# Performance work log

Hardware: AMD Instinct MI355X
Metric: run time of the kernel (lower is better)

The kernel has to match this reference:

```python
import jax, jax.numpy as jnp
import numpy as np

DIM = 768
HEADS = 12
HEAD_DIM = DIM // HEADS
SCALE = HEAD_DIM ** -0.5


def setup_inputs() -> dict:
    key = jax.random.key(0)
    ks = jax.random.split(key, 6)
    B, N = 4, 2048
    x = jax.random.normal(ks[0], (B, N, DIM), dtype=jnp.float32)
    s = DIM ** -0.5
    Wq = jax.random.normal(ks[1], (DIM, DIM), dtype=jnp.float32) * s
    Wk = jax.random.normal(ks[2], (DIM, DIM), dtype=jnp.float32) * s
    Wv = jax.random.normal(ks[3], (DIM, DIM), dtype=jnp.float32) * s
    Wp = jax.random.normal(ks[4], (DIM, DIM), dtype=jnp.float32) * s
    bp = jnp.zeros((DIM,), dtype=jnp.float32)
    return {"x": x, "Wq": Wq, "Wk": Wk, "Wv": Wv, "Wp": Wp, "bp": bp}


def reference(x, Wq, Wk, Wv, Wp, bp):
    B, N, C = x.shape
    # separate Q/K/V linears (no bias, qkv_bias=False); torch Linear: x @ W.T
    q = (x @ Wq.T).reshape(B, N, HEADS, HEAD_DIM).transpose(0, 2, 1, 3)
    k = (x @ Wk.T).reshape(B, N, HEADS, HEAD_DIM).transpose(0, 2, 1, 3)
    v = (x @ Wv.T).reshape(B, N, HEADS, HEAD_DIM).transpose(0, 2, 1, 3)
    # explicit full [B,H,N,N] attention matrix, as in the source
    attn = jnp.einsum("bhqd,bhkd->bhqk", q, k) * SCALE
    attn = jax.nn.softmax(attn, axis=-1)
    out = jnp.einsum("bhqk,bhkd->bhqd", attn, v)
    out = out.transpose(0, 2, 1, 3).reshape(B, N, C)
    return out @ Wp.T + bp
```

## Files before the change

kernel.cpp:

```cpp
#include <hip/hip_runtime.h>
#include <cstdint>

#define DIM   768
#define HEADS 12
#define HDIM  64
#define BATCH 4
#define SEQ   2048
#define MROWS (BATCH*SEQ)

typedef __bf16 bf16;
typedef __bf16 bf16x4_t __attribute__((ext_vector_type(4)));
typedef __bf16 bf16x8_t __attribute__((ext_vector_type(8)));
typedef float  f32x4_t  __attribute__((ext_vector_type(4)));
typedef float  f32x16_t __attribute__((ext_vector_type(16)));
typedef unsigned int u32x4_t __attribute__((ext_vector_type(4)));
typedef unsigned int u32x2_t __attribute__((ext_vector_type(2)));

__global__ void cast_bf16_kernel(const float* __restrict__ src, bf16* __restrict__ dst, int n4) {
    int i = blockIdx.x * blockDim.x + threadIdx.x;
    if (i >= n4) return;
    const float4 v = reinterpret_cast<const float4*>(src)[i];
    bf16x4_t o;
    o[0] = (bf16)v.x; o[1] = (bf16)v.y; o[2] = (bf16)v.z; o[3] = (bf16)v.w;
    reinterpret_cast<bf16x4_t*>(dst)[i] = o;
}

__global__ void cast_w4_kernel(const float* __restrict__ s0, const float* __restrict__ s1,
                               const float* __restrict__ s2, const float* __restrict__ s3,
                               bf16* __restrict__ d0, bf16* __restrict__ d1,
                               bf16* __restrict__ d2, bf16* __restrict__ d3, int n4) {
    int i = blockIdx.x * blockDim.x + threadIdx.x;
    if (i >= n4) return;
    int y = blockIdx.y;
    const float* src = (y == 0) ? s0 : (y == 1) ? s1 : (y == 2) ? s2 : s3;
    bf16* dst        = (y == 0) ? d0 : (y == 1) ? d1 : (y == 2) ? d2 : d3;
    const float4 v = reinterpret_cast<const float4*>(src)[i];
    bf16x4_t o;
    o[0] = (bf16)v.x; o[1] = (bf16)v.y; o[2] = (bf16)v.z; o[3] = (bf16)v.w;
    reinterpret_cast<bf16x4_t*>(dst)[i] = o;
}

__device__ __forceinline__ void gload_lds16(const bf16* g, bf16* l) {
    __builtin_amdgcn_global_load_lds((const __attribute__((address_space(1))) void*)g,
                                     (__attribute__((address_space(3))) void*)l, 16, 0, 0);
}

__global__ __launch_bounds__(256, 3) void qkvv_gemm(
        const bf16* __restrict__ X,
        const bf16* __restrict__ Wq, const bf16* __restrict__ Wk, const bf16* __restrict__ Wv,
        bf16* __restrict__ Q, bf16* __restrict__ Kd, bf16* __restrict__ Vt)
{
    __shared__ __align__(16) bf16 SM[128 * 128];
    bf16* As = SM;
    bf16* Bs = SM + 128 * 64;
    const int tid  = threadIdx.x;

    const int d  = blockIdx.x + 6 * blockIdx.y + 384 * blockIdx.z;
    const int L  = (d & 7) * 144 + (d >> 3);
    const int z  = L / 384;
    const int rem = L % 384;
    const int m0 = (rem % 6) * 128;
    const int n0 = (rem / 6) * 128;

    const bf16* Ap = (z == 0) ? Wq : (z == 1 ? Wk : Wv);
    const int lane = tid & 63;
    const int w    = tid >> 6;
    const int wm   = (w & 1) * 64, wn = (w >> 1) * 64;
    const int lr   = lane & 15, quad = lane >> 4;

    f32x4_t acc[4][4] = {};

    for (int kk = 0; kk < DIM; kk += 64) {
        #pragma unroll
        for (int i = 0; i < 4; ++i) {
            int c = tid + i * 256;
            int row = c >> 3, ch = c & 7;
            int gch = ch ^ (row & 7);
            gload_lds16(Ap + (size_t)(m0 + row) * DIM + kk + gch * 8, &As[row * 64 + ch * 8]);
            gload_lds16(X  + (size_t)(n0 + row) * DIM + kk + gch * 8, &Bs[row * 64 + ch * 8]);
        }
        __syncthreads();
        #pragma unroll
        for (int ks = 0; ks < 2; ++ks) {
            bf16x8_t af[4], bfr[4];
            #pragma unroll
            for (int i = 0; i < 4; ++i) {
                int row = wm + i * 16 + lr;
                int ch = (ks * 4 + quad) ^ (row & 7);
                af[i] = *reinterpret_cast<const bf16x8_t*>(&As[row * 64 + ch * 8]);
            }
            #pragma unroll
            for (int j = 0; j < 4; ++j) {
                int row = wn + j * 16 + lr;
                int ch = (ks * 4 + quad) ^ (row & 7);
                bfr[j] = *reinterpret_cast<const bf16x8_t*>(&Bs[row * 64 + ch * 8]);
            }
            #pragma unroll
            for (int i = 0; i < 4; ++i)
                #pragma unroll
                for (int j = 0; j < 4; ++j)
                    acc[i][j] = __builtin_amdgcn_mfma_f32_16x16x32_bf16(af[i], bfr[j], acc[i][j], 0, 0, 0);
        }
        __syncthreads();
    }

    if (z == 2) {
        #pragma unroll
        for (int i = 0; i < 4; ++i) {
            int ml = wm + i * 16 + quad * 4;
            #pragma unroll
            for (int j = 0; j < 4; ++j) {
                int nl = wn + j * 16 + lr;
                #pragma unroll
                for (int r = 0; r < 4; ++r)
                    SM[(ml + r) * 128 + nl] = (bf16)acc[i][j][r];
            }
        }
        __syncthreads();
        const int rr = tid >> 4, cc = tid & 15;
        #pragma unroll
        for (int rnd = 0; rnd < 8; ++rnd) {
            int ml = rnd * 16 + rr;
            *reinterpret_cast<bf16x8_t*>(&Vt[(size_t)(m0 + ml) * MROWS + n0 + cc * 8]) =
                *reinterpret_cast<const bf16x8_t*>(&SM[ml * 128 + cc * 8]);
        }
    } else {
        const float sc = (z == 0) ? 0.18033688011112042f : 1.0f;
        bf16* dst = (z == 0) ? Q : Kd;
        #pragma unroll
        for (int i = 0; i < 4; ++i) {
            int mb = m0 + wm + i * 16 + quad * 4;
            int h  = mb >> 6, d0 = mb & 63;
            #pragma unroll
            for (int j = 0; j < 4; ++j) {
                int sample = n0 + wn + j * 16 + lr;
                int b = sample >> 11, srow = sample & 2047;
                bf16x4_t o;
                #pragma unroll
                for (int r = 0; r < 4; ++r)
                    o[r] = (bf16)(acc[i][j][r] * sc);
                *reinterpret_cast<bf16x4_t*>(
                    &dst[(((size_t)b * HEADS + h) * SEQ + srow) * HDIM + d0]) = o;
            }
        }
    }
}

__global__ __launch_bounds__(256, 4) void out_gemm(
        const bf16* __restrict__ A,
        const bf16* __restrict__ W,
        const float* __restrict__ bias,
        float* __restrict__ out)
{
    __shared__ __align__(16) bf16 As[64*64];
    __shared__ __align__(16) bf16 Bs[128*64];
    const int tid  = threadIdx.x;

    const int d  = blockIdx.x + 6 * blockIdx.y;
    const int L  = (d & 7) * 96 + (d >> 3);
    const int n0 = (L % 6) * 128;
    const int m0 = (L / 6) * 64;

    const int lane = tid & 63;
    const int w    = tid >> 6;
    const int wm   = (w & 1) * 32, wn = (w >> 1) * 64;
    const int lr   = lane & 15, quad = lane >> 4;

    f32x4_t acc[2][4] = {};

    for (int kk = 0; kk < DIM; kk += 64) {
        #pragma unroll
        for (int i = 0; i < 2; ++i) {
            int c = tid + i * 256;
            int row = c >> 3, ch = c & 7;
            int gch = ch ^ (row & 7);
            gload_lds16(A + (size_t)(m0 + row) * DIM + kk + gch * 8, &As[row * 64 + ch * 8]);
        }
        #pragma unroll
        for (int i = 0; i < 4; ++i) {
            int c = tid + i * 256;
            int row = c >> 3, ch = c & 7;
            int gch = ch ^ (row & 7);
            gload_lds16(W + (size_t)(n0 + row) * DIM + kk + gch * 8, &Bs[row * 64 + ch * 8]);
        }
        __syncthreads();
        #pragma unroll
        for (int ks = 0; ks < 2; ++ks) {
            bf16x8_t af[2], bfr[4];
            #pragma unroll
            for (int i = 0; i < 2; ++i) {
                int row = wm + i * 16 + lr;
                int ch = (ks * 4 + quad) ^ (row & 7);
                af[i] = *reinterpret_cast<const bf16x8_t*>(&As[row * 64 + ch * 8]);
            }
            #pragma unroll
            for (int j = 0; j < 4; ++j) {
                int row = wn + j * 16 + lr;
                int ch = (ks * 4 + quad) ^ (row & 7);
                bfr[j] = *reinterpret_cast<const bf16x8_t*>(&Bs[row * 64 + ch * 8]);
            }
            #pragma unroll
            for (int i = 0; i < 2; ++i)
                #pragma unroll
                for (int j = 0; j < 4; ++j)
                    acc[i][j] = __builtin_amdgcn_mfma_f32_16x16x32_bf16(af[i], bfr[j], acc[i][j], 0, 0, 0);
        }
        __syncthreads();
    }

    #pragma unroll
    for (int i = 0; i < 2; ++i) {
        int mbase = m0 + wm + i * 16 + quad * 4;
        #pragma unroll
        for (int j = 0; j < 4; ++j) {
            int n = n0 + wn + j * 16 + lr;
            float bv = bias[n];
            #pragma unroll
            for (int r = 0; r < 4; ++r) {
                int m = mbase + r;
                out[(size_t)m * DIM + n] = acc[i][j][r] + bv;
            }
        }
    }
}

__global__ __launch_bounds__(256, 3) void attn_kernel(
        const bf16* __restrict__ Q, const bf16* __restrict__ Kd,
        const bf16* __restrict__ Vt, bf16* __restrict__ Ab)
{
    __shared__ __align__(16) bf16 KV[2][2][64*64];

    const int tid  = threadIdx.x;

    const int dd = blockIdx.x + 16 * blockIdx.y;
    const int L  = (dd & 7) * 96 + (dd >> 3);
    const int bh = L >> 4;
    const int q0 = (L & 15) * 128;

    const int b    = bh / HEADS, h = bh % HEADS;
    const int lane = tid & 63, w = tid >> 6;
    const int l31  = lane & 31, hw = lane >> 5;
    const int wq   = w * 32;

    const size_t qkbase = (size_t)bh * SEQ * HDIM;
    const size_t vbase  = (size_t)h * HDIM * MROWS + (size_t)b * SEQ;

    const int src_row = tid >> 3, src_ch = tid & 7;
    const int src_gch = src_ch ^ (src_row & 7);
    const int src_row2 = (tid + 256) >> 3, src_ch2 = tid & 7;
    const int src_gch2 = src_ch2 ^ (src_row2 & 7);

    {
        bf16* Qst = &KV[1][0][0];
        #pragma unroll
        for (int i = 0; i < 4; ++i) {
            int c = tid + i * 256;
            int row = c >> 3, ch = c & 7;
            int gch = ch ^ (row & 7);
            gload_lds16(Q + qkbase + (size_t)(q0 + row) * HDIM + gch * 8, &Qst[row * 64 + ch * 8]);
        }
    }

    const bf16* kp1 = Kd + qkbase + (size_t)src_row  * HDIM + src_gch  * 8;
    const bf16* kp2 = Kd + qkbase + (size_t)src_row2 * HDIM + src_gch2 * 8;
    const bf16* vp1 = Vt + vbase  + (size_t)src_row  * MROWS + src_gch  * 8;
    const bf16* vp2 = Vt + vbase  + (size_t)src_row2 * MROWS + src_gch2 * 8;
    bf16* kl1 = &KV[0][0][src_row  * 64 + src_ch  * 8];
    bf16* kl2 = &KV[0][0][src_row2 * 64 + src_ch2 * 8];
    bf16* vl1 = &KV[0][1][src_row  * 64 + src_ch  * 8];
    bf16* vl2 = &KV[0][1][src_row2 * 64 + src_ch2 * 8];
    const ptrdiff_t kstep = 64 * HDIM, vstep = 64;
    const ptrdiff_t lstep = 2 * 64 * 64;

    gload_lds16(kp1, kl1); gload_lds16(kp2, kl2);
    gload_lds16(vp1, vl1); gload_lds16(vp2, vl2);
    __syncthreads();

    bf16x8_t qf[4];
    {
        const bf16* Qst = &KV[1][0][0];
        int row = wq + l31;
        #pragma unroll
        for (int g = 0; g < 4; ++g) {
            int ch = (2 * g + hw) ^ (row & 7);
            qf[g] = *reinterpret_cast<const bf16x8_t*>(&Qst[row * 64 + ch * 8]);
        }
    }
    __syncthreads();

    f32x16_t oacc[2] = {};
    f32x16_t rsacc  = {};
    bf16x8_t ones8;
    #pragma unroll
    for (int i = 0; i < 8; ++i) ones8[i] = (bf16)1.0f;

    for (int it = 0; it < SEQ / 64; ++it) {
        const int buf = it & 1;
        if (it + 1 < SEQ / 64) {
            const ptrdiff_t g = (ptrdiff_t)(it + 1);
            const ptrdiff_t l = (buf ^ 1) ? lstep : 0;
            gload_lds16(kp1 + g * kstep, kl1 + l); gload_lds16(kp2 + g * kstep, kl2 + l);
            gload_lds16(vp1 + g * vstep, vl1 + l); gload_lds16(vp2 + g * vstep, vl2 + l);
        }

        const bf16* Ks = &KV[buf][0][0];
        const bf16* Vs = &KV[buf][1][0];

        f32x16_t sacc[2] = {};
        __builtin_amdgcn_s_setprio(1);
        #pragma unroll
        for (int kc = 0; kc < 2; ++kc) {
            int row = kc * 32 + l31;
            #pragma unroll
            for (int g = 0; g < 4; ++g) {
                int ch = (2 * g + hw) ^ (row & 7);
                bf16x8_t af = *reinterpret_cast<const bf16x8_t*>(&Ks[row * 64 + ch * 8]);
                sacc[kc] = __builtin_amdgcn_mfma_f32_32x32x16_bf16(af, qf[g], sacc[kc], 0, 0, 0);
            }
        }
        __builtin_amdgcn_s_setprio(0);

        bf16x8_t pk[4];
        #pragma unroll
        for (int kg = 0; kg < 4; ++kg) {
            #pragma unroll
            for (int j = 0; j < 8; ++j)
                pk[kg][j] = (bf16)__builtin_amdgcn_exp2f(sacc[kg >> 1][(kg & 1) * 8 + j]);
        }

        __builtin_amdgcn_s_setprio(1);
        #pragma unroll
        for (int kg = 0; kg < 4; ++kg)
            rsacc = __builtin_amdgcn_mfma_f32_32x32x16_bf16(pk[kg], ones8, rsacc, 0, 0, 0);

        #pragma unroll
        for (int dc = 0; dc < 2; ++dc) {
            int row = dc * 32 + l31;
            #pragma unroll
            for (int kg = 0; kg < 4; ++kg) {
                int myc = (2 * kg + hw) ^ (row & 7);
                union { u32x4_t i; bf16x8_t v; } u;
                u.i = *reinterpret_cast<const u32x4_t*>(&Vs[row * 64 + myc * 8]);
                u32x2_t r02 = __builtin_amdgcn_permlane32_swap(u.i[0], u.i[2], false, false);
                u32x2_t r13 = __builtin_amdgcn_permlane32_swap(u.i[1], u.i[3], false, false);
                u.i[0] = r02[0]; u.i[2] = r02[1];
                u.i[1] = r13[0]; u.i[3] = r13[1];
                oacc[dc] = __builtin_amdgcn_mfma_f32_32x32x16_bf16(pk[kg], u.v, oacc[dc], 0, 0, 0);
            }
        }
        __builtin_amdgcn_s_setprio(0);
        __syncthreads();
    }

    float inv[16];
    #pragma unroll
    for (int r = 0; r < 16; ++r)
        inv[r] = 1.0f / rsacc[r];
    #pragma unroll
    for (int dc = 0; dc < 2; ++dc) {
        int d = dc * 32 + l31;
        #pragma unroll
        for (int r = 0; r < 16; ++r) {
            int q = q0 + wq + (r & 3) + 8 * (r >> 2) + 4 * hw;
            Ab[((size_t)b * SEQ + q) * DIM + h * HDIM + d] = (bf16)(oacc[dc][r] * inv[r]);
        }
    }
}

extern "C" void kernel_launch(void* const* d_in, const int* in_sizes, int n_in,
                              void* d_out, int out_size, void* d_ws, size_t ws_size,
                              hipStream_t stream) {
    (void)in_sizes; (void)n_in; (void)out_size; (void)ws_size;
    const float* x  = (const float*)d_in[0];
    const float* Wq = (const float*)d_in[1];
    const float* Wk = (const float*)d_in[2];
    const float* Wv = (const float*)d_in[3];
    const float* Wp = (const float*)d_in[4];
    const float* bp = (const float*)d_in[5];
    float* out = (float*)d_out;

    char* ws = (char*)d_ws;
    size_t off = 0;
    auto alloc = [&](size_t bytes) {
        void* p = ws + off;
        off += (bytes + 255) & ~(size_t)255;
        return p;
    };
    const size_t big = (size_t)MROWS * DIM * sizeof(bf16);
    const size_t wsz = (size_t)DIM * DIM * sizeof(bf16);
    bf16* Xb  = (bf16*)alloc(big);
    bf16* Qb  = (bf16*)alloc(big);
    bf16* Kb  = (bf16*)alloc(big);
    bf16* Vtb = (bf16*)alloc(big);
    bf16* Wqb = (bf16*)alloc(wsz);
    bf16* Wkb = (bf16*)alloc(wsz);
    bf16* Wvb = (bf16*)alloc(wsz);
    bf16* Wpb = (bf16*)alloc(wsz);
    bf16* Ab  = Xb;

    const int x4 = MROWS * DIM / 4;
    cast_bf16_kernel<<<(x4 + 255) / 256, 256, 0, stream>>>(x, Xb, x4);
    const int w4 = DIM * DIM / 4;
    cast_w4_kernel<<<dim3((w4 + 255) / 256, 4), 256, 0, stream>>>(
        Wq, Wk, Wv, Wp, Wqb, Wkb, Wvb, Wpb, w4);

    qkvv_gemm<<<dim3(DIM / 128, MROWS / 128, 3), 256, 0, stream>>>(
        Xb, Wqb, Wkb, Wvb, Qb, Kb, Vtb);

    attn_kernel<<<dim3(SEQ / 128, BATCH * HEADS), 256, 0, stream>>>(Qb, Kb, Vtb, Ab);

    out_gemm<<<dim3(DIM / 128, MROWS / 64), 256, 0, stream>>>(Ab, Wpb, bp, out);
}
```

Measured before the change: 206.3 us.

## Software-pipeline PV MFMA behind next QK and pre-permute V layout

The attention loop is software-pipelined: the P·V and row-sum MFMAs for the previous tile now run right after the current tile's QK^T MFMAs, so exp2 work can overlap matrix work. V gets a triple-buffered LDS region (Q staging moved into the fifth slot) to hold the previous tile alive. The QKV projection epilogue writes V^T columns in a permuted order, which removes the permlane32_swap shuffles in the attention inner loop. This raises LDS use and register pressure, and correctness depends on the epilogue permutation matching the old swap.

After: 206.2 us. Within noise of the previous version (-0.1%).

```diff
diff --git a/kernel.cpp b/kernel.cpp
--- a/kernel.cpp
+++ b/kernel.cpp
@@ -13,8 +13,6 @@
 typedef __bf16 bf16x8_t __attribute__((ext_vector_type(8)));
 typedef float  f32x4_t  __attribute__((ext_vector_type(4)));
 typedef float  f32x16_t __attribute__((ext_vector_type(16)));
-typedef unsigned int u32x4_t __attribute__((ext_vector_type(4)));
-typedef unsigned int u32x2_t __attribute__((ext_vector_type(2)));
 
 __global__ void cast_bf16_kernel(const float* __restrict__ src, bf16* __restrict__ dst, int n4) {
     int i = blockIdx.x * blockDim.x + threadIdx.x;
@@ -110,7 +108,9 @@
             int ml = wm + i * 16 + quad * 4;
             #pragma unroll
             for (int j = 0; j < 4; ++j) {
-                int nl = wn + j * 16 + lr;
+                int p   = lr >> 2;
+                int pp  = ((p & 1) << 1) | (p >> 1);
+                int nl  = wn + j * 16 + (pp << 2) + (lr & 3);
                 #pragma unroll
                 for (int r = 0; r < 4; ++r)
                     SM[(ml + r) * 128 + nl] = (bf16)acc[i][j][r];
@@ -228,7 +228,9 @@
         const bf16* __restrict__ Q, const bf16* __restrict__ Kd,
         const bf16* __restrict__ Vt, bf16* __restrict__ Ab)
 {
-    __shared__ __align__(16) bf16 KV[2][2][64*64];
+    __shared__ __align__(16) bf16 SH[5 * 64 * 64];
+    bf16* Kb = SH;
+    bf16* Vb = SH + 2 * 4096;
 
     const int tid  = threadIdx.x;
 
@@ -245,19 +247,21 @@
     const size_t qkbase = (size_t)bh * SEQ * HDIM;
     const size_t vbase  = (size_t)h * HDIM * MROWS + (size_t)b * SEQ;
 
-    const int src_row = tid >> 3, src_ch = tid & 7;
-    const int src_gch = src_ch ^ (src_row & 7);
-    const int src_row2 = (tid + 256) >> 3, src_ch2 = tid & 7;
-    const int src_gch2 = src_ch2 ^ (src_row2 & 7);
+    const int src_row  = tid >> 3, src_ch = tid & 7;
+    const int src_gch  = src_ch ^ (src_row & 7);
+    const int src_row2 = (tid + 256) >> 3;
+    const int src_gch2 = src_ch ^ (src_row2 & 7);
+    const int loff1 = src_row  * 64 + src_ch * 8;
+    const int loff2 = src_row2 * 64 + src_ch * 8;
 
     {
-        bf16* Qst = &KV[1][0][0];
+        bf16* Qst = Vb + 4096;
         #pragma unroll
         for (int i = 0; i < 4; ++i) {
             int c = tid + i * 256;
             int row = c >> 3, ch = c & 7;
             int gch = ch ^ (row & 7);
-            gload_lds16(Q + qkbase + (size_t)(q0 + row) * HDIM + gch * 8, &Qst[row * 64 + ch * 8]);
+            gload_lds16(Q + qkbase + (size_t)(q0 + row) * HDIM + gch * 8, Qst + row * 64 + ch * 8);
         }
     }
 
@@ -265,20 +269,15 @@
     const bf16* kp2 = Kd + qkbase + (size_t)src_row2 * HDIM + src_gch2 * 8;
     const bf16* vp1 = Vt + vbase  + (size_t)src_row  * MROWS + src_gch  * 8;
     const bf16* vp2 = Vt + vbase  + (size_t)src_row2 * MROWS + src_gch2 * 8;
-    bf16* kl1 = &KV[0][0][src_row  * 64 + src_ch  * 8];
-    bf16* kl2 = &KV[0][0][src_row2 * 64 + src_ch2 * 8];
-    bf16* vl1 = &KV[0][1][src_row  * 64 + src_ch  * 8];
-    bf16* vl2 = &KV[0][1][src_row2 * 64 + src_ch2 * 8];
     const ptrdiff_t kstep = 64 * HDIM, vstep = 64;
-    const ptrdiff_t lstep = 2 * 64 * 64;
-
-    gload_lds16(kp1, kl1); gload_lds16(kp2, kl2);
-    gload_lds16(vp1, vl1); gload_lds16(vp2, vl2);
+
+    gload_lds16(kp1, Kb + loff1); gload_lds16(kp2, Kb + loff2);
+    gload_lds16(vp1, Vb + loff1); gload_lds16(vp2, Vb + loff2);
     __syncthreads();
 
     bf16x8_t qf[4];
     {
-        const bf16* Qst = &KV[1][0][0];
+        const bf16* Qst = Vb + 4096;
         int row = wq + l31;
         #pragma unroll
         for (int g = 0; g < 4; ++g) {
@@ -290,21 +289,23 @@
 
     f32x16_t oacc[2] = {};
     f32x16_t rsacc  = {};
+    bf16x8_t pk[4];
     bf16x8_t ones8;
     #pragma unroll
     for (int i = 0; i < 8; ++i) ones8[i] = (bf16)1.0f;
 
+    int vprev = 2, vcur = 0, vnext = 1;
+
     for (int it = 0; it < SEQ / 64; ++it) {
-        const int buf = it & 1;
         if (it + 1 < SEQ / 64) {
             const ptrdiff_t g = (ptrdiff_t)(it + 1);
-            const ptrdiff_t l = (buf ^ 1) ? lstep : 0;
-            gload_lds16(kp1 + g * kstep, kl1 + l); gload_lds16(kp2 + g * kstep, kl2 + l);
-            gload_lds16(vp1 + g * vstep, vl1 + l); gload_lds16(vp2 + g * vstep, vl2 + l);
-        }
-
-        const bf16* Ks = &KV[buf][0][0];
-        const bf16* Vs = &KV[buf][1][0];
+            bf16* kd = Kb + ((it + 1) & 1) * 4096;
+            bf16* vd = Vb + vnext * 4096;
+            gload_lds16(kp1 + g * kstep, kd + loff1); gload_lds16(kp2 + g * kstep, kd + loff2);
+            gload_lds16(vp1 + g * vstep, vd + loff1); gload_lds16(vp2 + g * vstep, vd + loff2);
+        }
+
+        const bf16* Ks = Kb + (it & 1) * 4096;
 
         f32x16_t sacc[2] = {};
         __builtin_amdgcn_s_setprio(1);
@@ -318,9 +319,25 @@
                 sacc[kc] = __builtin_amdgcn_mfma_f32_32x32x16_bf16(af, qf[g], sacc[kc], 0, 0, 0);
             }
         }
+
+        if (it > 0) {
+            const bf16* Vs = Vb + vprev * 4096;
+            #pragma unroll
+            for (int dc = 0; dc < 2; ++dc) {
+                int row = dc * 32 + l31;
+                #pragma unroll
+                for (int kg = 0; kg < 4; ++kg) {
+                    int myc = (2 * kg + hw) ^ (row & 7);
+                    bf16x8_t bb = *reinterpret_cast<const bf16x8_t*>(&Vs[row * 64 + myc * 8]);
+                    oacc[dc] = __builtin_amdgcn_mfma_f32_32x32x16_bf16(pk[kg], bb, oacc[dc], 0, 0, 0);
+                }
+            }
+            #pragma unroll
+            for (int kg = 0; kg < 4; ++kg)
+                rsacc = __builtin_amdgcn_mfma_f32_32x32x16_bf16(pk[kg], ones8, rsacc, 0, 0, 0);
+        }
         __builtin_amdgcn_s_setprio(0);
 
-        bf16x8_t pk[4];
         #pragma unroll
         for (int kg = 0; kg < 4; ++kg) {
             #pragma unroll
@@ -328,28 +345,25 @@
                 pk[kg][j] = (bf16)__builtin_amdgcn_exp2f(sacc[kg >> 1][(kg & 1) * 8 + j]);
         }
 
-        __builtin_amdgcn_s_setprio(1);
+        __syncthreads();
+        int tmp = vprev; vprev = vcur; vcur = vnext; vnext = tmp;
+    }
+
+    {
+        const bf16* Vs = Vb + vprev * 4096;
+        #pragma unroll
+        for (int dc = 0; dc < 2; ++dc) {
+            int row = dc * 32 + l31;
+            #pragma unroll
+            for (int kg = 0; kg < 4; ++kg) {
+                int myc = (2 * kg + hw) ^ (row & 7);
+                bf16x8_t bb = *reinterpret_cast<const bf16x8_t*>(&Vs[row * 64 + myc * 8]);
+                oacc[dc] = __builtin_amdgcn_mfma_f32_32x32x16_bf16(pk[kg], bb, oacc[dc], 0, 0, 0);
+            }
+        }
         #pragma unroll
         for (int kg = 0; kg < 4; ++kg)
             rsacc = __builtin_amdgcn_mfma_f32_32x32x16_bf16(pk[kg], ones8, rsacc, 0, 0, 0);
-
-        #pragma unroll
-        for (int dc = 0; dc < 2; ++dc) {
-            int row = dc * 32 + l31;
-            #pragma unroll
-            for (int kg = 0; kg < 4; ++kg) {
-                int myc = (2 * kg + hw) ^ (row & 7);
-                union { u32x4_t i; bf16x8_t v; } u;
-                u.i = *reinterpret_cast<const u32x4_t*>(&Vs[row * 64 + myc * 8]);
-                u32x2_t r02 = __builtin_amdgcn_permlane32_swap(u.i[0], u.i[2], false, false);
-                u32x2_t r13 = __builtin_amdgcn_permlane32_swap(u.i[1], u.i[3], false, false);
-                u.i[0] = r02[0]; u.i[2] = r02[1];
-                u.i[1] = r13[0]; u.i[3] = r13[1];
-                oacc[dc] = __builtin_amdgcn_mfma_f32_32x32x16_bf16(pk[kg], u.v, oacc[dc], 0, 0, 0);
-            }
-        }
-        __builtin_amdgcn_s_setprio(0);
-        __syncthreads();
     }
 
     float inv[16];
```
